# Kernel optimization log

Hardware: AMD Instinct MI355X
Metric: run time of the kernel (lower is better)

The kernel has to match this reference:

```python
import jax, jax.numpy as jnp
import numpy as np

D_MODEL = 256
NUM_HEAD = 4
D_HEAD = D_MODEL // NUM_HEAD
B, N, M = 1, 512, 512


def setup_inputs() -> dict:
    key = jax.random.key(0)
    ks = jax.random.split(key, 13)
    s = 1.0 / np.sqrt(D_MODEL)
    inp = {
        'input_q': jax.random.normal(ks[0], (B, N, D_MODEL), jnp.float32),
        'input_k': jax.random.normal(ks[1], (B, M, D_MODEL), jnp.float32),
        'input_v': jax.random.normal(ks[2], (B, M, D_MODEL), jnp.float32),
        'input_p': jax.random.normal(ks[3], (B, N, M, D_MODEL), jnp.float32),
        'key_masks': jnp.zeros((B, M), dtype=bool),
        'Wq': jax.random.normal(ks[4], (D_MODEL, D_MODEL), jnp.float32) * s,
        'bq': jnp.zeros((D_MODEL,), jnp.float32),
        'Wk': jax.random.normal(ks[5], (D_MODEL, D_MODEL), jnp.float32) * s,
        'bk': jnp.zeros((D_MODEL,), jnp.float32),
        'Wv': jax.random.normal(ks[6], (D_MODEL, D_MODEL), jnp.float32) * s,
        'bv': jnp.zeros((D_MODEL,), jnp.float32),
        'Wp': jax.random.normal(ks[7], (D_MODEL, D_MODEL), jnp.float32) * s,
        'bp': jnp.zeros((D_MODEL,), jnp.float32),
    }
    return inp


def reference(input_q, input_k, input_v, input_p, key_masks,
              Wq, bq, Wk, bk, Wv, bv, Wp, bp):
    H, Dh = NUM_HEAD, D_HEAD
    b, n, _ = input_q.shape
    m = input_k.shape[1]
    # linear projections (PyTorch Linear: x @ W.T + b)
    q = (input_q @ Wq.T + bq).reshape(b, n, H, Dh).transpose(0, 2, 1, 3)   # (B,H,N,Dh)
    k = (input_k @ Wk.T + bk).reshape(b, m, H, Dh).transpose(0, 2, 1, 3)   # (B,H,M,Dh)
    v = (input_v @ Wv.T + bv).reshape(b, m, H, Dh).transpose(0, 2, 1, 3)   # (B,H,M,Dh)
    p = (input_p @ Wp.T + bp).reshape(b, n, m, H, Dh)                      # (B,N,M,H,Dh)
    # content scores + per-pair RPE scores (q dot p)
    scores = (jnp.einsum('bhnd,bhmd->bhnm', q, k)
              + jnp.einsum('bhnd,bnmhd->bhnm', q, p)) / np.sqrt(Dh)
    scores = jnp.where(key_masks[:, None, None, :], -jnp.inf, scores)
    attn = jax.nn.softmax(scores, axis=-1)                                 # (B,H,N,M)
    hidden = jnp.einsum('bhnm,bhmd->bhnd', attn, v)
    hidden = hidden.transpose(0, 2, 1, 3).reshape(b, n, H * Dh)            # (B,N,C)
    return hidden
```

## Files before the change

### kernel.cpp

```cpp
#include <hip/hip_runtime.h>
#include <math.h>

#define DMODEL 256
#define NSEQ   512
#define MSEQ   512

#define WS_Q      0
#define WS_K      131072
#define WS_V      262144
#define WS_WPE    393216
#define WS_SQK    917504

typedef float v4f __attribute__((ext_vector_type(4)));

__global__ __launch_bounds__(256) void proj_qkv(
    const float* __restrict__ xq, const float* __restrict__ xk,
    const float* __restrict__ xv,
    const float* __restrict__ Wq, const float* __restrict__ bq,
    const float* __restrict__ Wk, const float* __restrict__ bk,
    const float* __restrict__ Wv, const float* __restrict__ bv,
    float* __restrict__ ws)
{
    int bid = blockIdx.x;
    int mat = bid >> 6;
    int rb  = bid & 63;
    const float* X; const float* W; const float* b; float* Y;
    if (mat == 0)      { X = xq; W = Wq; b = bq; Y = ws + WS_Q; }
    else if (mat == 1) { X = xk; W = Wk; b = bk; Y = ws + WS_K; }
    else               { X = xv; W = Wv; b = bv; Y = ws + WS_V; }

    int c  = threadIdx.x;
    int r0 = rb * 8;
    float acc[8];
    float bias = b[c];
#pragma unroll
    for (int r = 0; r < 8; ++r) acc[r] = bias;

    const float4* Wrow = (const float4*)(W + (size_t)c * DMODEL);
    for (int d4 = 0; d4 < 64; ++d4) {
        float4 w = Wrow[d4];
#pragma unroll
        for (int r = 0; r < 8; ++r) {
            float4 x = ((const float4*)(X + (size_t)(r0 + r) * DMODEL))[d4];
            acc[r] += w.x * x.x + w.y * x.y + w.z * x.z + w.w * x.w;
        }
    }
#pragma unroll
    for (int r = 0; r < 8; ++r)
        Y[(size_t)(r0 + r) * DMODEL + c] = acc[r];
}

__global__ __launch_bounds__(256) void make_wpeff(
    const float* __restrict__ Wp, float* __restrict__ ws)
{
    const float* q   = ws + WS_Q;
    float*       wpe = ws + WS_WPE;
    int n = blockIdx.x;
    int d = threadIdx.x;

    __shared__ float ql[256];
    ql[d] = q[(size_t)n * DMODEL + d];
    __syncthreads();

    float acc[4];
#pragma unroll
    for (int h = 0; h < 4; ++h) {
        float a = 0.f;
#pragma unroll 8
        for (int dh = 0; dh < 64; ++dh) {
            int c = h * 64 + dh;
            a += ql[c] * Wp[(size_t)c * DMODEL + d];
        }
        acc[h] = a;
    }
    *(float4*)&wpe[(size_t)n * 1024 + d * 4] =
        make_float4(acc[0], acc[1], acc[2], acc[3]);
}

__global__ __launch_bounds__(256) void qk_scores(
    const float* __restrict__ bp, float* __restrict__ ws)
{
    const float* q   = ws + WS_Q;
    const float* k   = ws + WS_K;
    float*       sqk = ws + WS_SQK;

    int bid = blockIdx.x;
    int h   = bid >> 6;
    int g   = bid & 63;
    int n0  = g * 8;
    int tid = threadIdx.x;

    __shared__ float qls[8][64];
    __shared__ float qb[8];

    if (tid < 128) {
        int row = tid >> 4, col = (tid & 15) * 4;
        *(float4*)&qls[row][col] =
            *(const float4*)&q[(size_t)(n0 + row) * DMODEL + h * 64 + col];
    }
    __syncthreads();
    if (tid < 8) {
        float s = 0.f;
        for (int dh = 0; dh < 64; ++dh) s += qls[tid][dh] * bp[h * 64 + dh];
        qb[tid] = s;
    }
    __syncthreads();

    const float* ka = k + (size_t)tid * DMODEL + h * 64;
    const float* kb = ka + (size_t)256 * DMODEL;
    float acca[8] = {};
    float accb[8] = {};
#pragma unroll 4
    for (int d4 = 0; d4 < 16; ++d4) {
        float4 xa = *(const float4*)(ka + d4 * 4);
        float4 xb = *(const float4*)(kb + d4 * 4);
#pragma unroll
        for (int j = 0; j < 8; ++j) {
            float4 qq = *(const float4*)&qls[j][d4 * 4];
            acca[j] += xa.x * qq.x + xa.y * qq.y + xa.z * qq.z + xa.w * qq.w;
            accb[j] += xb.x * qq.x + xb.y * qq.y + xb.z * qq.z + xb.w * qq.w;
        }
    }
#pragma unroll
    for (int j = 0; j < 8; ++j) {
        size_t base = (size_t)h * 262144 + (size_t)(n0 + j) * MSEQ;
        sqk[base + tid]       = 0.125f * (acca[j] + qb[j]);
        sqk[base + tid + 256] = 0.125f * (accb[j] + qb[j]);
    }
}

__global__ __launch_bounds__(256) void p_scores(
    const float* __restrict__ Xp, float* __restrict__ ws)
{
    const float* wpe = ws + WS_WPE;
    float*       sqk = ws + WS_SQK;

    int n = blockIdx.x >> 1;
    int m = (blockIdx.x & 1) * 256 + threadIdx.x;

    __shared__ float4 wl[256];
    wl[threadIdx.x] = ((const float4*)(wpe + (size_t)n * 1024))[threadIdx.x];
    __syncthreads();

    const v4f* __restrict__ xrow =
        (const v4f*)(Xp + ((size_t)n * MSEQ + m) * DMODEL);

    v4f xa[16], xb[16];
#pragma unroll
    for (int i = 0; i < 16; ++i) xa[i] = xrow[i];
#pragma unroll
    for (int i = 0; i < 16; ++i) xb[i] = xrow[16 + i];

    float s0 = 0.f, s1 = 0.f, s2 = 0.f, s3 = 0.f;

    auto consume = [&](const v4f* cur, int base) {
#pragma unroll
        for (int i = 0; i < 16; ++i) {
            int d4 = base + i;
            v4f x = cur[i];
            float4 w0 = wl[d4 * 4 + 0];
            float4 w1 = wl[d4 * 4 + 1];
            float4 w2 = wl[d4 * 4 + 2];
            float4 w3 = wl[d4 * 4 + 3];
            s0 += x.x * w0.x + x.y * w1.x + x.z * w2.x + x.w * w3.x;
            s1 += x.x * w0.y + x.y * w1.y + x.z * w2.y + x.w * w3.y;
            s2 += x.x * w0.z + x.y * w1.z + x.z * w2.z + x.w * w3.z;
            s3 += x.x * w0.w + x.y * w1.w + x.z * w2.w + x.w * w3.w;
        }
    };

    consume(xa, 0);
#pragma unroll
    for (int i = 0; i < 16; ++i) xa[i] = xrow[32 + i];
    consume(xb, 16);
#pragma unroll
    for (int i = 0; i < 16; ++i) xb[i] = xrow[48 + i];
    consume(xa, 32);
    consume(xb, 48);

    size_t ob = (size_t)n * MSEQ + m;
    sqk[0 * 262144 + ob] += 0.125f * s0;
    sqk[1 * 262144 + ob] += 0.125f * s1;
    sqk[2 * 262144 + ob] += 0.125f * s2;
    sqk[3 * 262144 + ob] += 0.125f * s3;
}

__global__ __launch_bounds__(256) void softmax_av(
    const unsigned char* __restrict__ mask,
    float* __restrict__ out, float* __restrict__ ws)
{
    const float* v      = ws + WS_V;
    const float* scores = ws + WS_SQK;

    int bid = blockIdx.x;
    int h   = bid >> 6;
    int g   = bid & 63;
    int n0  = g * 8;

    __shared__ float  pl[MSEQ * 8];
    __shared__ float4 red4[256];
    __shared__ float  wred[4];

    int tid  = threadIdx.x;
    int lane = tid & 63, wv = tid >> 6;

    for (int j = 0; j < 8; ++j) {
        int n = n0 + j;
        const float* srow = scores + (size_t)h * 262144 + (size_t)n * MSEQ;
        float s0 = srow[tid];
        float s1 = srow[tid + 256];
        if (mask[tid])       s0 = -INFINITY;
        if (mask[tid + 256]) s1 = -INFINITY;

        float mx = fmaxf(s0, s1);
#pragma unroll
        for (int off = 32; off; off >>= 1) mx = fmaxf(mx, __shfl_xor(mx, off));
        if (lane == 0) wred[wv] = mx;
        __syncthreads();
        mx = fmaxf(fmaxf(wred[0], wred[1]), fmaxf(wred[2], wred[3]));

        float e0 = __expf(s0 - mx);
        float e1 = __expf(s1 - mx);
        float sm = e0 + e1;
#pragma unroll
        for (int off = 32; off; off >>= 1) sm += __shfl_xor(sm, off);
        __syncthreads();
        if (lane == 0) wred[wv] = sm;
        __syncthreads();
        sm = wred[0] + wred[1] + wred[2] + wred[3];
        float rinv = 1.0f / sm;

        pl[(size_t)tid * 8 + j]         = e0 * rinv;
        pl[(size_t)(tid + 256) * 8 + j] = e1 * rinv;
        __syncthreads();
    }

    int dhq = tid & 15, mq = tid >> 4;
    float acc[8][4] = {};
    for (int i = 0; i < 32; ++i) {
        int m = mq * 32 + i;
        float4 vv = *(const float4*)&v[(size_t)m * DMODEL + h * 64 + dhq * 4];
        float4 pa = *(const float4*)&pl[m * 8];
        float4 pb = *(const float4*)&pl[m * 8 + 4];
#pragma unroll
        for (int j = 0; j < 4; ++j) {
            float pv = (&pa.x)[j];
            acc[j][0] += pv * vv.x; acc[j][1] += pv * vv.y;
            acc[j][2] += pv * vv.z; acc[j][3] += pv * vv.w;
        }
#pragma unroll
        for (int j = 0; j < 4; ++j) {
            float pv = (&pb.x)[j];
            acc[4 + j][0] += pv * vv.x; acc[4 + j][1] += pv * vv.y;
            acc[4 + j][2] += pv * vv.z; acc[4 + j][3] += pv * vv.w;
        }
    }

    for (int j = 0; j < 8; ++j) {
        red4[mq * 16 + dhq] =
            make_float4(acc[j][0], acc[j][1], acc[j][2], acc[j][3]);
        __syncthreads();
        if (tid < 64) {
            int dq = tid >> 2, x = tid & 3;
            float s = 0.f;
#pragma unroll
            for (int qq = 0; qq < 16; ++qq)
                s += ((const float*)&red4[qq * 16 + dq])[x];
            out[(size_t)(n0 + j) * DMODEL + h * 64 + tid] = s;
        }
        __syncthreads();
    }
}

extern "C" void kernel_launch(void* const* d_in, const int* in_sizes, int n_in,
                              void* d_out, int out_size, void* d_ws,
                              size_t ws_size, hipStream_t stream)
{
    const float* xq = (const float*)d_in[0];
    const float* xk = (const float*)d_in[1];
    const float* xv = (const float*)d_in[2];
    const float* xp = (const float*)d_in[3];
    const unsigned char* mask = (const unsigned char*)d_in[4];
    const float* Wq = (const float*)d_in[5];
    const float* bq = (const float*)d_in[6];
    const float* Wk = (const float*)d_in[7];
    const float* bk = (const float*)d_in[8];
    const float* Wv = (const float*)d_in[9];
    const float* bv = (const float*)d_in[10];
    const float* Wp = (const float*)d_in[11];
    const float* bp = (const float*)d_in[12];
    float* out = (float*)d_out;
    float* ws  = (float*)d_ws;

    proj_qkv  <<<192,  256, 0, stream>>>(xq, xk, xv, Wq, bq, Wk, bk, Wv, bv, ws);
    make_wpeff<<<512,  256, 0, stream>>>(Wp, ws);
    qk_scores <<<256,  256, 0, stream>>>(bp, ws);
    p_scores  <<<1024, 256, 0, stream>>>(xp, ws);
    softmax_av<<<256,  256, 0, stream>>>(mask, out, ws);
}
```

Before: 119.6 us.

## Stream input_p rows via async global-to-LDS loads with wave-level reductions

Rewrites p_scores so each wave handles 32 rows of input_p. Rows are staged into LDS with global_load_lds direct copies, double-buffered, with manual vmcnt waits, so each row is read with fully coalesced 16-byte lane accesses instead of one thread walking a whole row. Each lane keeps its slice of the effective weight in registers, and dot products are reduced across the wave with xor shuffles. The grid is doubled. This adds 24 shuffle-add steps per row and depends on the vmcnt counts being correct for the asynchronous copies.

```diff
diff --git a/kernel.cpp b/kernel.cpp
--- a/kernel.cpp
+++ b/kernel.cpp
@@ -135,54 +135,91 @@
     const float* wpe = ws + WS_WPE;
     float*       sqk = ws + WS_SQK;
 
-    int n = blockIdx.x >> 1;
-    int m = (blockIdx.x & 1) * 256 + threadIdx.x;
-
-    __shared__ float4 wl[256];
-    wl[threadIdx.x] = ((const float4*)(wpe + (size_t)n * 1024))[threadIdx.x];
+    int n    = blockIdx.x >> 2;
+    int m0   = (blockIdx.x & 3) * 128;
+    int tid  = threadIdx.x;
+    int wv   = tid >> 6;
+    int lane = tid & 63;
+
+    __shared__ float xs[4][2][2048];
+    __shared__ float smv[4][128];
+
+    const float4* wp4 = (const float4*)(wpe + (size_t)n * 1024);
+    float4 wreg[4];
+#pragma unroll
+    for (int c = 0; c < 4; ++c) wreg[c] = wp4[lane * 4 + c];
+
+    const float* gbase = Xp + ((size_t)n * MSEQ + m0 + wv * 32) * DMODEL;
+
+#define STAGE(cc, bb)                                                         \
+    {                                                                         \
+        _Pragma("unroll")                                                     \
+        for (int r = 0; r < 8; ++r) {                                         \
+            const float* g = gbase + ((cc) * 8 + r) * DMODEL + lane * 4;      \
+            float* l = &xs[wv][bb][r * 256];                                  \
+            __builtin_amdgcn_global_load_lds(                                 \
+                (const __attribute__((address_space(1))) unsigned int*)g,     \
+                (__attribute__((address_space(3))) unsigned int*)l, 16, 0, 0);\
+        }                                                                     \
+    }
+
+#define CONSUME(cc, bb)                                                       \
+    {                                                                         \
+        _Pragma("unroll")                                                     \
+        for (int r = 0; r < 8; ++r) {                                         \
+            v4f x = *(const v4f*)&xs[wv][bb][r * 256 + lane * 4];             \
+            float p0 = x.x*wreg[0].x + x.y*wreg[1].x + x.z*wreg[2].x + x.w*wreg[3].x; \
+            float p1 = x.x*wreg[0].y + x.y*wreg[1].y + x.z*wreg[2].y + x.w*wreg[3].y; \
+            float p2 = x.x*wreg[0].z + x.y*wreg[1].z + x.z*wreg[2].z + x.w*wreg[3].z; \
+            float p3 = x.x*wreg[0].w + x.y*wreg[1].w + x.z*wreg[2].w + x.w*wreg[3].w; \
+            _Pragma("unroll")                                                 \
+            for (int off = 1; off < 64; off <<= 1) {                          \
+                p0 += __shfl_xor(p0, off);                                    \
+                p1 += __shfl_xor(p1, off);                                    \
+                p2 += __shfl_xor(p2, off);                                    \
+                p3 += __shfl_xor(p3, off);                                    \
+            }                                                                 \
+            if (lane == 0) {                                                  \
+                int ml = wv * 32 + (cc) * 8 + r;                              \
+                smv[0][ml] = p0; smv[1][ml] = p1;                             \
+                smv[2][ml] = p2; smv[3][ml] = p3;                             \
+            }                                                                 \
+        }                                                                     \
+    }
+
+    STAGE(0, 0)
+    STAGE(1, 1)
+
+    asm volatile("s_waitcnt vmcnt(8)" ::: "memory");
+    __builtin_amdgcn_sched_barrier(0);
+    CONSUME(0, 0)
+    __builtin_amdgcn_sched_barrier(0);
+    STAGE(2, 0)
+
+    asm volatile("s_waitcnt vmcnt(8)" ::: "memory");
+    __builtin_amdgcn_sched_barrier(0);
+    CONSUME(1, 1)
+    __builtin_amdgcn_sched_barrier(0);
+    STAGE(3, 1)
+
+    asm volatile("s_waitcnt vmcnt(8)" ::: "memory");
+    __builtin_amdgcn_sched_barrier(0);
+    CONSUME(2, 0)
+
+    asm volatile("s_waitcnt vmcnt(0)" ::: "memory");
+    __builtin_amdgcn_sched_barrier(0);
+    CONSUME(3, 1)
+
+#undef STAGE
+#undef CONSUME
+
     __syncthreads();
-
-    const v4f* __restrict__ xrow =
-        (const v4f*)(Xp + ((size_t)n * MSEQ + m) * DMODEL);
-
-    v4f xa[16], xb[16];
-#pragma unroll
-    for (int i = 0; i < 16; ++i) xa[i] = xrow[i];
-#pragma unroll
-    for (int i = 0; i < 16; ++i) xb[i] = xrow[16 + i];
-
-    float s0 = 0.f, s1 = 0.f, s2 = 0.f, s3 = 0.f;
-
-    auto consume = [&](const v4f* cur, int base) {
-#pragma unroll
-        for (int i = 0; i < 16; ++i) {
-            int d4 = base + i;
-            v4f x = cur[i];
-            float4 w0 = wl[d4 * 4 + 0];
-            float4 w1 = wl[d4 * 4 + 1];
-            float4 w2 = wl[d4 * 4 + 2];
-            float4 w3 = wl[d4 * 4 + 3];
-            s0 += x.x * w0.x + x.y * w1.x + x.z * w2.x + x.w * w3.x;
-            s1 += x.x * w0.y + x.y * w1.y + x.z * w2.y + x.w * w3.y;
-            s2 += x.x * w0.z + x.y * w1.z + x.z * w2.z + x.w * w3.z;
-            s3 += x.x * w0.w + x.y * w1.w + x.z * w2.w + x.w * w3.w;
-        }
-    };
-
-    consume(xa, 0);
-#pragma unroll
-    for (int i = 0; i < 16; ++i) xa[i] = xrow[32 + i];
-    consume(xb, 16);
-#pragma unroll
-    for (int i = 0; i < 16; ++i) xb[i] = xrow[48 + i];
-    consume(xa, 32);
-    consume(xb, 48);
-
-    size_t ob = (size_t)n * MSEQ + m;
-    sqk[0 * 262144 + ob] += 0.125f * s0;
-    sqk[1 * 262144 + ob] += 0.125f * s1;
-    sqk[2 * 262144 + ob] += 0.125f * s2;
-    sqk[3 * 262144 + ob] += 0.125f * s3;
+    if (tid < 128) {
+        size_t ob = (size_t)n * MSEQ + m0 + tid;
+#pragma unroll
+        for (int h = 0; h < 4; ++h)
+            sqk[h * 262144 + ob] += 0.125f * smv[h][tid];
+    }
 }
 
 __global__ __launch_bounds__(256) void softmax_av(
@@ -295,6 +332,6 @@
     proj_qkv  <<<192,  256, 0, stream>>>(xq, xk, xv, Wq, bq, Wk, bk, Wv, bv, ws);
     make_wpeff<<<512,  256, 0, stream>>>(Wp, ws);
     qk_scores <<<256,  256, 0, stream>>>(bp, ws);
-    p_scores  <<<1024, 256, 0, stream>>>(xp, ws);
+    p_scores  <<<2048, 256, 0, stream>>>(xp, ws);
     softmax_av<<<256,  256, 0, stream>>>(mask, out, ws);
 }
```

After: 157.2 us. 31.4% more time.

## Merge wpeff and qk kernels into one launch; simplify p_scores loop

Applied to the files above, without the earlier changes.

Combines the effective-Wp kernel and the QK score kernel into a single launch, with block ranges split by blockIdx, so one launch and its serialization gap disappear. The wpeff half now computes two rows per block, reusing each Wp load for both and reading q straight from global memory instead of LDS. p_scores drops its manual double-buffered register prefetch for a simple unrolled loop. That lowers register pressure and may raise occupancy, but it depends on the compiler to hide load latency on the dominant 256 MB streaming read.

```diff
diff --git a/kernel.cpp b/kernel.cpp
--- a/kernel.cpp
+++ b/kernel.cpp
@@ -50,82 +50,85 @@
         Y[(size_t)(r0 + r) * DMODEL + c] = acc[r];
 }
 
-__global__ __launch_bounds__(256) void make_wpeff(
-    const float* __restrict__ Wp, float* __restrict__ ws)
-{
-    const float* q   = ws + WS_Q;
-    float*       wpe = ws + WS_WPE;
-    int n = blockIdx.x;
-    int d = threadIdx.x;
-
-    __shared__ float ql[256];
-    ql[d] = q[(size_t)n * DMODEL + d];
-    __syncthreads();
-
-    float acc[4];
-#pragma unroll
-    for (int h = 0; h < 4; ++h) {
-        float a = 0.f;
+__global__ __launch_bounds__(256) void wpeff_qk(
+    const float* __restrict__ Wp, const float* __restrict__ bp,
+    float* __restrict__ ws)
+{
+    int bid = blockIdx.x;
+    int tid = threadIdx.x;
+
+    if (bid < 256) {
+        const float* q   = ws + WS_Q;
+        float*       wpe = ws + WS_WPE;
+        int n0 = bid * 2;
+        int d  = tid;
+
+        const float* q0 = q + (size_t)n0 * DMODEL;
+        const float* q1 = q0 + DMODEL;
+
+        float acc0[4] = {0.f, 0.f, 0.f, 0.f};
+        float acc1[4] = {0.f, 0.f, 0.f, 0.f};
+#pragma unroll
+        for (int h = 0; h < 4; ++h) {
 #pragma unroll 8
-        for (int dh = 0; dh < 64; ++dh) {
-            int c = h * 64 + dh;
-            a += ql[c] * Wp[(size_t)c * DMODEL + d];
-        }
-        acc[h] = a;
-    }
-    *(float4*)&wpe[(size_t)n * 1024 + d * 4] =
-        make_float4(acc[0], acc[1], acc[2], acc[3]);
-}
-
-__global__ __launch_bounds__(256) void qk_scores(
-    const float* __restrict__ bp, float* __restrict__ ws)
-{
-    const float* q   = ws + WS_Q;
-    const float* k   = ws + WS_K;
-    float*       sqk = ws + WS_SQK;
-
-    int bid = blockIdx.x;
-    int h   = bid >> 6;
-    int g   = bid & 63;
-    int n0  = g * 8;
-    int tid = threadIdx.x;
-
-    __shared__ float qls[8][64];
-    __shared__ float qb[8];
-
-    if (tid < 128) {
-        int row = tid >> 4, col = (tid & 15) * 4;
-        *(float4*)&qls[row][col] =
-            *(const float4*)&q[(size_t)(n0 + row) * DMODEL + h * 64 + col];
-    }
-    __syncthreads();
-    if (tid < 8) {
-        float s = 0.f;
-        for (int dh = 0; dh < 64; ++dh) s += qls[tid][dh] * bp[h * 64 + dh];
-        qb[tid] = s;
-    }
-    __syncthreads();
-
-    const float* ka = k + (size_t)tid * DMODEL + h * 64;
-    const float* kb = ka + (size_t)256 * DMODEL;
-    float acca[8] = {};
-    float accb[8] = {};
+            for (int dh = 0; dh < 64; ++dh) {
+                int c = h * 64 + dh;
+                float w = Wp[(size_t)c * DMODEL + d];
+                acc0[h] += q0[c] * w;
+                acc1[h] += q1[c] * w;
+            }
+        }
+        *(float4*)&wpe[(size_t)n0 * 1024 + d * 4] =
+            make_float4(acc0[0], acc0[1], acc0[2], acc0[3]);
+        *(float4*)&wpe[(size_t)(n0 + 1) * 1024 + d * 4] =
+            make_float4(acc1[0], acc1[1], acc1[2], acc1[3]);
+    } else {
+        const float* q   = ws + WS_Q;
+        const float* k   = ws + WS_K;
+        float*       sqk = ws + WS_SQK;
+
+        int b2  = bid - 256;
+        int h   = b2 >> 6;
+        int g   = b2 & 63;
+        int n0  = g * 8;
+
+        __shared__ float qls[8][64];
+        __shared__ float qb[8];
+
+        if (tid < 128) {
+            int row = tid >> 4, col = (tid & 15) * 4;
+            *(float4*)&qls[row][col] =
+                *(const float4*)&q[(size_t)(n0 + row) * DMODEL + h * 64 + col];
+        }
+        __syncthreads();
+        if (tid < 8) {
+            float s = 0.f;
+            for (int dh = 0; dh < 64; ++dh) s += qls[tid][dh] * bp[h * 64 + dh];
+            qb[tid] = s;
+        }
+        __syncthreads();
+
+        const float* ka = k + (size_t)tid * DMODEL + h * 64;
+        const float* kb = ka + (size_t)256 * DMODEL;
+        float acca[8] = {};
+        float accb[8] = {};
 #pragma unroll 4
-    for (int d4 = 0; d4 < 16; ++d4) {
-        float4 xa = *(const float4*)(ka + d4 * 4);
-        float4 xb = *(const float4*)(kb + d4 * 4);
+        for (int d4 = 0; d4 < 16; ++d4) {
+            float4 xa = *(const float4*)(ka + d4 * 4);
+            float4 xb = *(const float4*)(kb + d4 * 4);
+#pragma unroll
+            for (int j = 0; j < 8; ++j) {
+                float4 qq = *(const float4*)&qls[j][d4 * 4];
+                acca[j] += xa.x * qq.x + xa.y * qq.y + xa.z * qq.z + xa.w * qq.w;
+                accb[j] += xb.x * qq.x + xb.y * qq.y + xb.z * qq.z + xb.w * qq.w;
+            }
+        }
 #pragma unroll
         for (int j = 0; j < 8; ++j) {
-            float4 qq = *(const float4*)&qls[j][d4 * 4];
-            acca[j] += xa.x * qq.x + xa.y * qq.y + xa.z * qq.z + xa.w * qq.w;
-            accb[j] += xb.x * qq.x + xb.y * qq.y + xb.z * qq.z + xb.w * qq.w;
-        }
-    }
-#pragma unroll
-    for (int j = 0; j < 8; ++j) {
-        size_t base = (size_t)h * 262144 + (size_t)(n0 + j) * MSEQ;
-        sqk[base + tid]       = 0.125f * (acca[j] + qb[j]);
-        sqk[base + tid + 256] = 0.125f * (accb[j] + qb[j]);
+            size_t base = (size_t)h * 262144 + (size_t)(n0 + j) * MSEQ;
+            sqk[base + tid]       = 0.125f * (acca[j] + qb[j]);
+            sqk[base + tid + 256] = 0.125f * (accb[j] + qb[j]);
+        }
     }
 }
 
@@ -142,47 +145,26 @@
     wl[threadIdx.x] = ((const float4*)(wpe + (size_t)n * 1024))[threadIdx.x];
     __syncthreads();
 
-    const v4f* __restrict__ xrow =
-        (const v4f*)(Xp + ((size_t)n * MSEQ + m) * DMODEL);
-
-    v4f xa[16], xb[16];
-#pragma unroll
-    for (int i = 0; i < 16; ++i) xa[i] = xrow[i];
-#pragma unroll
-    for (int i = 0; i < 16; ++i) xb[i] = xrow[16 + i];
-
-    float s0 = 0.f, s1 = 0.f, s2 = 0.f, s3 = 0.f;
-
-    auto consume = [&](const v4f* cur, int base) {
-#pragma unroll
-        for (int i = 0; i < 16; ++i) {
-            int d4 = base + i;
-            v4f x = cur[i];
-            float4 w0 = wl[d4 * 4 + 0];
-            float4 w1 = wl[d4 * 4 + 1];
-            float4 w2 = wl[d4 * 4 + 2];
-            float4 w3 = wl[d4 * 4 + 3];
-            s0 += x.x * w0.x + x.y * w1.x + x.z * w2.x + x.w * w3.x;
-            s1 += x.x * w0.y + x.y * w1.y + x.z * w2.y + x.w * w3.y;
-            s2 += x.x * w0.z + x.y * w1.z + x.z * w2.z + x.w * w3.z;
-            s3 += x.x * w0.w + x.y * w1.w + x.z * w2.w + x.w * w3.w;
-        }
-    };
-
-    consume(xa, 0);
-#pragma unroll
-    for (int i = 0; i < 16; ++i) xa[i] = xrow[32 + i];
-    consume(xb, 16);
-#pragma unroll
-    for (int i = 0; i < 16; ++i) xb[i] = xrow[48 + i];
-    consume(xa, 32);
-    consume(xb, 48);
-
+    const float4* xrow =
+        (const float4*)(Xp + (size_t)((size_t)n * MSEQ + m) * DMODEL);
+    float4 acc = make_float4(0.f, 0.f, 0.f, 0.f);
+#pragma unroll 8
+    for (int d4 = 0; d4 < 64; ++d4) {
+        float4 x  = xrow[d4];
+        float4 w0 = wl[d4 * 4 + 0];
+        float4 w1 = wl[d4 * 4 + 1];
+        float4 w2 = wl[d4 * 4 + 2];
+        float4 w3 = wl[d4 * 4 + 3];
+        acc.x += x.x * w0.x + x.y * w1.x + x.z * w2.x + x.w * w3.x;
+        acc.y += x.x * w0.y + x.y * w1.y + x.z * w2.y + x.w * w3.y;
+        acc.z += x.x * w0.z + x.y * w1.z + x.z * w2.z + x.w * w3.z;
+        acc.w += x.x * w0.w + x.y * w1.w + x.z * w2.w + x.w * w3.w;
+    }
     size_t ob = (size_t)n * MSEQ + m;
-    sqk[0 * 262144 + ob] += 0.125f * s0;
-    sqk[1 * 262144 + ob] += 0.125f * s1;
-    sqk[2 * 262144 + ob] += 0.125f * s2;
-    sqk[3 * 262144 + ob] += 0.125f * s3;
+    sqk[0 * 262144 + ob] += 0.125f * acc.x;
+    sqk[1 * 262144 + ob] += 0.125f * acc.y;
+    sqk[2 * 262144 + ob] += 0.125f * acc.z;
+    sqk[3 * 262144 + ob] += 0.125f * acc.w;
 }
 
 __global__ __launch_bounds__(256) void softmax_av(
@@ -293,8 +275,7 @@
     float* ws  = (float*)d_ws;
 
     proj_qkv  <<<192,  256, 0, stream>>>(xq, xk, xv, Wq, bq, Wk, bk, Wv, bv, ws);
-    make_wpeff<<<512,  256, 0, stream>>>(Wp, ws);
-    qk_scores <<<256,  256, 0, stream>>>(bp, ws);
+    wpeff_qk  <<<512,  256, 0, stream>>>(Wp, bp, ws);
     p_scores  <<<1024, 256, 0, stream>>>(xp, ws);
     softmax_av<<<256,  256, 0, stream>>>(mask, out, ws);
 }
```

Result: faster. 99.51 us (-16.8%).
